# Performance work log

Measured on AMD Instinct MI355X. Metric: run time of the kernel, lower is better.

Reference implementation:

```python
import jax, jax.numpy as jnp
import numpy as np

E, H, FF = 1024, 16, 4096
HD = E // H
B, S = 4, 2048


def _ln(x, g, b, eps=1e-5):
    m = jnp.mean(x, axis=-1, keepdims=True)
    v = jnp.mean((x - m) ** 2, axis=-1, keepdims=True)
    return (x - m) / jnp.sqrt(v + eps) * g + b


def setup_inputs() -> dict:
    k = jax.random.key(0)
    ks = jax.random.split(k, 12)
    sd = 0.02
    return {
        "value": jax.random.normal(ks[0], (B, S, E), jnp.float32),
        "key": jax.random.normal(ks[1], (B, S, E), jnp.float32),
        "query": jax.random.normal(ks[2], (B, S, E), jnp.float32),
        "mask": jnp.ones((B, 1, 1, S), jnp.int32),
        "Wv": sd * jax.random.normal(ks[3], (E, E), jnp.float32),
        "Wk": sd * jax.random.normal(ks[4], (E, E), jnp.float32),
        "Wq": sd * jax.random.normal(ks[5], (E, E), jnp.float32),
        "Wo": sd * jax.random.normal(ks[6], (E, E), jnp.float32),
        "bo": jnp.zeros((E,), jnp.float32),
        "ln1_g": jnp.ones((E,), jnp.float32), "ln1_b": jnp.zeros((E,), jnp.float32),
        "ln2_g": jnp.ones((E,), jnp.float32), "ln2_b": jnp.zeros((E,), jnp.float32),
        "lnf_g": jnp.ones((E,), jnp.float32), "lnf_b": jnp.zeros((E,), jnp.float32),
        "W1": sd * jax.random.normal(ks[7], (E, FF), jnp.float32),
        "b1": jnp.zeros((FF,), jnp.float32),
        "W2": sd * jax.random.normal(ks[8], (FF, E), jnp.float32),
        "b2": jnp.zeros((E,), jnp.float32),
    }


def reference(value, key, query, mask, Wv, Wk, Wq, Wo, bo,
              ln1_g, ln1_b, ln2_g, ln2_b, lnf_g, lnf_b, W1, b1, W2, b2):
    N, Sq, Em = query.shape
    # pre-norms (value & key share prenorm2 params, as in the torch module)
    v = _ln(value, ln2_g, ln2_b)
    k = _ln(key, ln2_g, ln2_b)
    q = _ln(query, ln1_g, ln1_b)
    # QKV projections (no bias), split heads
    V = (v @ Wv).reshape(N, v.shape[1], H, HD)
    K = (k @ Wk).reshape(N, k.shape[1], H, HD)
    Q = (q @ Wq).reshape(N, Sq, H, HD)
    energy = jnp.einsum("nqhd,nkhd->nhqk", Q, K)  # [N,H,Sq,Sk]
    energy = jnp.where(mask == 0, jnp.float32(-1e20), energy)
    attn = jax.nn.softmax(energy / jnp.float32(HD ** 0.5), axis=-1)
    out = jnp.einsum("nhqk,nkhd->nqhd", attn, V).reshape(N, Sq, Em)
    out = out @ Wo + bo
    x = out + q  # residual (drop_path is identity in eval)
    f = _ln(x, lnf_g, lnf_b) @ W1 + b1
    f = jax.nn.gelu(f, approximate=False) @ W2 + b2
    return f + x
```

## Files before the change

### kernel.cpp

```cpp
#include <hip/hip_runtime.h>
#include <hip/hip_bf16.h>
#include <math.h>

typedef __bf16 bf16x8 __attribute__((ext_vector_type(8)));
typedef __bf16 bf16x4 __attribute__((ext_vector_type(4)));
typedef float f32x4 __attribute__((ext_vector_type(4)));

#define AS1 __attribute__((address_space(1)))
#define AS3 __attribute__((address_space(3)))

__device__ __forceinline__ void gll16(const __bf16* g, __bf16* l) {
    __builtin_amdgcn_global_load_lds((const AS1 unsigned int*)g,
                                     (AS3 unsigned int*)l, 16, 0, 0);
}

__device__ __forceinline__ unsigned pkbf(float a, float b) {
    union { __bf16 h[2]; unsigned u; } t;
    t.h[0] = (__bf16)a; t.h[1] = (__bf16)b;
    return t.u;
}

__global__ __launch_bounds__(256) void transpose_all(
    const float* __restrict__ Wq, const float* __restrict__ Wk,
    const float* __restrict__ Wv, const float* __restrict__ Wo,
    const float* __restrict__ W1, const float* __restrict__ W2,
    __bf16* __restrict__ Wqt, __bf16* __restrict__ Wkt,
    __bf16* __restrict__ Wvt, __bf16* __restrict__ Wot,
    __bf16* __restrict__ W1t, __bf16* __restrict__ W2t) {
    int g = blockIdx.x;
    const float* W; __bf16* Wt; int K, N, kt, nt;
    if (g < 4096) {
        int mi = g >> 10, loc = g & 1023;
        K = 1024; N = 1024; kt = loc >> 5; nt = loc & 31;
        W  = mi == 0 ? Wq  : mi == 1 ? Wk  : mi == 2 ? Wv  : Wo;
        Wt = mi == 0 ? Wqt : mi == 1 ? Wkt : mi == 2 ? Wvt : Wot;
    } else if (g < 8192) {
        int loc = g - 4096; W = W1; Wt = W1t;
        K = 1024; N = 4096; kt = loc >> 7; nt = loc & 127;
    } else {
        int loc = g - 8192; W = W2; Wt = W2t;
        K = 4096; N = 1024; kt = loc >> 5; nt = loc & 31;
    }
    int k0 = kt * 32, n0 = nt * 32;
    __shared__ float tile[32][33];
    int tx = threadIdx.x & 31, ty = threadIdx.x >> 5;
    #pragma unroll
    for (int j = ty; j < 32; j += 8)
        tile[j][tx] = W[(size_t)(k0 + j) * N + n0 + tx];
    __syncthreads();
    #pragma unroll
    for (int j = ty; j < 32; j += 8)
        Wt[(size_t)(n0 + j) * K + k0 + tx] = (__bf16)tile[tx][j];
}

__global__ __launch_bounds__(256) void ln3_kernel(
    const float* __restrict__ q, const float* __restrict__ k,
    const float* __restrict__ v,
    const float* __restrict__ g1, const float* __restrict__ b1,
    const float* __restrict__ g2, const float* __restrict__ b2,
    float* __restrict__ qln, __bf16* __restrict__ qbf,
    __bf16* __restrict__ kbf, __bf16* __restrict__ vbf) {
    const int E = 1024;
    int which = blockIdx.y;
    const float* x = which == 0 ? q : which == 1 ? k : v;
    const float* g = which == 0 ? g1 : g2;
    const float* bb = which == 0 ? b1 : b2;
    float* o32 = which == 0 ? qln : nullptr;
    __bf16* obf = which == 0 ? qbf : which == 1 ? kbf : vbf;

    size_t row = blockIdx.x;
    int t = threadIdx.x;
    float4 val = ((const float4*)(x + row * E))[t];
    float s  = val.x + val.y + val.z + val.w;
    float s2 = val.x * val.x + val.y * val.y + val.z * val.z + val.w * val.w;
    #pragma unroll
    for (int off = 32; off >= 1; off >>= 1) {
        s  += __shfl_down(s, off);
        s2 += __shfl_down(s2, off);
    }
    __shared__ float red[2][4];
    int wid = t >> 6, lane = t & 63;
    if (lane == 0) { red[0][wid] = s; red[1][wid] = s2; }
    __syncthreads();
    if (t == 0) {
        float S1 = red[0][0] + red[0][1] + red[0][2] + red[0][3];
        float S2 = red[1][0] + red[1][1] + red[1][2] + red[1][3];
        float mean = S1 / E;
        float var  = S2 / E - mean * mean;
        red[0][0] = mean;
        red[1][0] = 1.0f / sqrtf(var + 1e-5f);
    }
    __syncthreads();
    float mean = red[0][0], rstd = red[1][0];
    float4 gv = ((const float4*)g)[t];
    float4 bv = ((const float4*)bb)[t];
    float y0 = (val.x - mean) * rstd * gv.x + bv.x;
    float y1 = (val.y - mean) * rstd * gv.y + bv.y;
    float y2 = (val.z - mean) * rstd * gv.z + bv.z;
    float y3 = (val.w - mean) * rstd * gv.w + bv.w;
    if (o32) ((float4*)(o32 + row * E))[t] = make_float4(y0, y1, y2, y3);
    bf16x4 o;
    o[0] = (__bf16)y0; o[1] = (__bf16)y1; o[2] = (__bf16)y2; o[3] = (__bf16)y3;
    ((bf16x4*)(obf + row * E))[t] = o;
}

__global__ __launch_bounds__(256) void ln_kernel(const float* __restrict__ x,
                                                 const float* __restrict__ g,
                                                 const float* __restrict__ bb,
                                                 __bf16* __restrict__ outbf) {
    const int E = 1024;
    size_t row = blockIdx.x;
    int t = threadIdx.x;
    float4 v = ((const float4*)(x + row * E))[t];
    float s  = v.x + v.y + v.z + v.w;
    float s2 = v.x * v.x + v.y * v.y + v.z * v.z + v.w * v.w;
    #pragma unroll
    for (int off = 32; off >= 1; off >>= 1) {
        s  += __shfl_down(s, off);
        s2 += __shfl_down(s2, off);
    }
    __shared__ float red[2][4];
    int wid = t >> 6, lane = t & 63;
    if (lane == 0) { red[0][wid] = s; red[1][wid] = s2; }
    __syncthreads();
    if (t == 0) {
        float S1 = red[0][0] + red[0][1] + red[0][2] + red[0][3];
        float S2 = red[1][0] + red[1][1] + red[1][2] + red[1][3];
        float mean = S1 / E;
        float var  = S2 / E - mean * mean;
        red[0][0] = mean;
        red[1][0] = 1.0f / sqrtf(var + 1e-5f);
    }
    __syncthreads();
    float mean = red[0][0], rstd = red[1][0];
    float4 gv = ((const float4*)g)[t];
    float4 bv = ((const float4*)bb)[t];
    bf16x4 o;
    o[0] = (__bf16)((v.x - mean) * rstd * gv.x + bv.x);
    o[1] = (__bf16)((v.y - mean) * rstd * gv.y + bv.y);
    o[2] = (__bf16)((v.z - mean) * rstd * gv.z + bv.z);
    o[3] = (__bf16)((v.w - mean) * rstd * gv.w + bv.w);
    ((bf16x4*)(outbf + row * E))[t] = o;
}

template <int EPI>
__global__ __launch_bounds__(256) void gemm128(const __bf16* __restrict__ A,
                                               const __bf16* __restrict__ A2,
                                               const __bf16* __restrict__ Bt,
                                               const __bf16* __restrict__ Bt2,
                                               const float* __restrict__ bias,
                                               const float* __restrict__ resid,
                                               void* __restrict__ Cout,
                                               int M, int N, int K,
                                               int splitN, float scale) {
    __shared__ __bf16 As[128 * 64];
    __shared__ __bf16 Bs[128 * 64];
    int tid  = threadIdx.x;
    int lane = tid & 63, wid = tid >> 6;
    int quad = lane >> 4, l15 = lane & 15;
    int waveM = wid >> 1, waveN = wid & 1;
    size_t rowBase = (size_t)blockIdx.y * 128;
    size_t colBase = (size_t)blockIdx.x * 128;

    const __bf16* Ap = A; const __bf16* Bp = Bt;
    size_t colLoc = colBase;
    float sc = scale;
    if ((int)colBase >= splitN) { Ap = A2; Bp = Bt2; colLoc = colBase - splitN; sc = 1.0f; }

    int lrow8  = lane >> 3;
    int lchunk = (lane & 7) ^ lrow8;
    const __bf16* Ag0 = Ap + (rowBase + wid * 32 + lrow8) * (size_t)K + lchunk * 8;
    const __bf16* Bg0 = Bp + (colLoc  + wid * 32 + lrow8) * (size_t)K + lchunk * 8;
    __bf16* AsB = &As[(wid * 32) * 64];
    __bf16* BsB = &Bs[(wid * 32) * 64];

    f32x4 acc[4][4] = {};
    int swz = l15 & 7;

    for (int kb = 0; kb < K; kb += 64) {
        __syncthreads();
        #pragma unroll
        for (int i = 0; i < 4; i++) {
            gll16(Ag0 + (size_t)i * 8 * K + kb, AsB + i * 512);
            gll16(Bg0 + (size_t)i * 8 * K + kb, BsB + i * 512);
        }
        __syncthreads();
        #pragma unroll
        for (int ks = 0; ks < 2; ks++) {
            int p = ((ks * 4 + quad) ^ swz) * 8;
            bf16x8 af[4], bfr[4];
            #pragma unroll
            for (int mi = 0; mi < 4; mi++)
                af[mi] = *(const bf16x8*)&As[(waveM * 64 + mi * 16 + l15) * 64 + p];
            #pragma unroll
            for (int ni = 0; ni < 4; ni++)
                bfr[ni] = *(const bf16x8*)&Bs[(waveN * 64 + ni * 16 + l15) * 64 + p];
            #pragma unroll
            for (int mi = 0; mi < 4; mi++)
                #pragma unroll
                for (int ni = 0; ni < 4; ni++)
                    acc[mi][ni] = __builtin_amdgcn_mfma_f32_16x16x32_bf16(
                        bfr[ni], af[mi], acc[mi][ni], 0, 0, 0);
        }
    }

    #pragma unroll
    for (int mi = 0; mi < 4; mi++)
    #pragma unroll
    for (int ni = 0; ni < 4; ni++) {
        size_t row = rowBase + waveM * 64 + mi * 16 + l15;
        size_t col = colBase + waveN * 64 + ni * 16 + quad * 4;
        f32x4 v = acc[mi][ni];
        if (EPI == 1) {
            float4 b4 = *(const float4*)&bias[col];
            float4 r4 = *(const float4*)&resid[row * N + col];
            float4 o;
            o.x = v[0] + b4.x + r4.x; o.y = v[1] + b4.y + r4.y;
            o.z = v[2] + b4.z + r4.z; o.w = v[3] + b4.w + r4.w;
            *(float4*)&((float*)Cout)[row * N + col] = o;
        } else if (EPI == 2) {
            float4 b4 = *(const float4*)&bias[col];
            bf16x4 pk;
            #pragma unroll
            for (int r = 0; r < 4; r++) {
                float t2 = v[r] + ((const float*)&b4)[r];
                pk[r] = (__bf16)(0.5f * t2 * (1.0f + erff(t2 * 0.70710678118654752f)));
            }
            *(bf16x4*)&((__bf16*)Cout)[row * N + col] = pk;
        } else {
            bf16x4 pk;
            #pragma unroll
            for (int r = 0; r < 4; r++) pk[r] = (__bf16)(v[r] * sc);
            *(bf16x4*)&((__bf16*)Cout)[row * N + col] = pk;
        }
    }
}

__global__ __launch_bounds__(256) void gemmV(const __bf16* __restrict__ A,
                                             const __bf16* __restrict__ Bt,
                                             __bf16* __restrict__ Cout,
                                             int M, int N, int K) {
    __shared__ __bf16 As[128 * 64];
    __shared__ __bf16 Bs[128 * 64];
    int tid  = threadIdx.x;
    int lane = tid & 63, wid = tid >> 6;
    int quad = lane >> 4, l15 = lane & 15;
    int waveM = wid >> 1, waveN = wid & 1;
    size_t rowBase = (size_t)blockIdx.y * 128;
    size_t colBase = (size_t)blockIdx.x * 128;

    int lrow8  = lane >> 3;
    int lchunk = (lane & 7) ^ lrow8;
    const __bf16* Ag0 = A  + (rowBase + wid * 32 + lrow8) * (size_t)K + lchunk * 8;
    const __bf16* Bg0 = Bt + (colBase + wid * 32 + lrow8) * (size_t)K + lchunk * 8;
    __bf16* AsB = &As[(wid * 32) * 64];
    __bf16* BsB = &Bs[(wid * 32) * 64];

    f32x4 acc[4][4] = {};
    int swz = l15 & 7;

    for (int kb = 0; kb < K; kb += 64) {
        __syncthreads();
        #pragma unroll
        for (int i = 0; i < 4; i++) {
            gll16(Ag0 + (size_t)i * 8 * K + kb, AsB + i * 512);
            gll16(Bg0 + (size_t)i * 8 * K + kb, BsB + i * 512);
        }
        __syncthreads();
        #pragma unroll
        for (int ks = 0; ks < 2; ks++) {
            int p = ((ks * 4 + quad) ^ swz) * 8;
            bf16x8 af[4], bfr[4];
            #pragma unroll
            for (int mi = 0; mi < 4; mi++)
                af[mi] = *(const bf16x8*)&As[(waveM * 64 + mi * 16 + l15) * 64 + p];
            #pragma unroll
            for (int ni = 0; ni < 4; ni++)
                bfr[ni] = *(const bf16x8*)&Bs[(waveN * 64 + ni * 16 + l15) * 64 + p];
            #pragma unroll
            for (int mi = 0; mi < 4; mi++)
                #pragma unroll
                for (int ni = 0; ni < 4; ni++)
                    acc[mi][ni] = __builtin_amdgcn_mfma_f32_16x16x32_bf16(
                        af[mi], bfr[ni], acc[mi][ni], 0, 0, 0);
        }
    }

    #pragma unroll
    for (int mi = 0; mi < 4; mi++)
    #pragma unroll
    for (int ni = 0; ni < 4; ni++) {
        size_t col = colBase + waveN * 64 + ni * 16 + l15;
        size_t m0  = rowBase + waveM * 64 + mi * 16 + quad * 4;
        bf16x4 pk;
        #pragma unroll
        for (int r = 0; r < 4; r++) pk[r] = (__bf16)acc[mi][ni][r];
        *(bf16x4*)&Cout[col * M + m0] = pk;
    }
}

__global__ __launch_bounds__(256) void attn_kernel(const __bf16* __restrict__ QK,
                                                   const __bf16* __restrict__ Vt,
                                                   const int* __restrict__ mask,
                                                   __bf16* __restrict__ Out) {
    const int S = 2048, E = 1024, E2 = 2048, M = 8192;
    int qt = blockIdx.x, bh = blockIdx.y;
    int b = bh >> 4, h = bh & 15;
    int q0 = qt * 128;
    int tid = threadIdx.x, lane = tid & 63, wid = tid >> 6;
    int quad = lane >> 4, l15 = lane & 15;

    __shared__ __bf16 KV[2][2 * 4096];

    bf16x8 aq[2][2];
    #pragma unroll
    for (int m = 0; m < 2; m++)
        #pragma unroll
        for (int hh = 0; hh < 2; hh++) {
            size_t row = (size_t)(b * S + q0 + wid * 32 + m * 16 + l15);
            aq[m][hh] = *(const bf16x8*)(QK + row * E2 + h * 64 + hh * 32 + quad * 8);
        }

    int lrow8  = lane >> 3;
    int lchunk = (lane & 7) ^ lrow8;
    const __bf16* Kg0 = QK + (size_t)(b * S + wid * 16 + lrow8) * E2 + 1024 + h * 64 + lchunk * 8;
    const __bf16* Vg0 = Vt + (size_t)(h * 64 + wid * 16 + lrow8) * M + b * S + lchunk * 8;

    int srcA = ((quad & 1) * 2) * 16 + l15;
    int srcB = srcA + 16;
    bool selHi = (quad >= 2);
    int swz = l15 & 7;

    f32x4 accO[2][4] = {};
    float accl[2] = {0.f, 0.f};

    {
        __bf16* Kd = &KV[0][(wid * 16) * 64];
        __bf16* Vd = &KV[0][4096 + (wid * 16) * 64];
        #pragma unroll
        for (int i = 0; i < 2; i++) {
            gll16(Kg0 + (size_t)i * 8 * E2, Kd + i * 512);
            gll16(Vg0 + (size_t)i * 8 * M,  Vd + i * 512);
        }
    }
    __syncthreads();

    for (int kt = 0; kt < S / 64; kt++) {
        int k0 = kt * 64;
        int buf = kt & 1;
        if (kt + 1 < S / 64) {
            int kn = k0 + 64;
            __bf16* Kd = &KV[buf ^ 1][(wid * 16) * 64];
            __bf16* Vd = &KV[buf ^ 1][4096 + (wid * 16) * 64];
            #pragma unroll
            for (int i = 0; i < 2; i++) {
                gll16(Kg0 + (size_t)(kn + i * 8) * E2, Kd + i * 512);
                gll16(Vg0 + (size_t)i * 8 * M + kn,    Vd + i * 512);
            }
        }
        const __bf16* Ksb = &KV[buf][0];
        const __bf16* Vsb = &KV[buf][4096];

        f32x4 sa[2][4];
        #pragma unroll
        for (int nt = 0; nt < 4; nt++) {
            bf16x8 a0 = *(const bf16x8*)&Ksb[(nt * 16 + l15) * 64 + ((0 * 4 + quad) ^ swz) * 8];
            bf16x8 a1 = *(const bf16x8*)&Ksb[(nt * 16 + l15) * 64 + ((1 * 4 + quad) ^ swz) * 8];
            #pragma unroll
            for (int m = 0; m < 2; m++) {
                f32x4 a = {};
                a = __builtin_amdgcn_mfma_f32_16x16x32_bf16(a0, aq[m][0], a, 0, 0, 0);
                a = __builtin_amdgcn_mfma_f32_16x16x32_bf16(a1, aq[m][1], a, 0, 0, 0);
                sa[m][nt] = a;
            }
        }

        unsigned pd[2][4][2];
        #pragma unroll
        for (int nt = 0; nt < 4; nt++) {
            int4 mz = *(const int4*)&mask[b * S + k0 + nt * 16 + quad * 4];
            #pragma unroll
            for (int m = 0; m < 2; m++) {
                float p0 = mz.x ? __expf(sa[m][nt][0]) : 0.f;
                float p1 = mz.y ? __expf(sa[m][nt][1]) : 0.f;
                float p2 = mz.z ? __expf(sa[m][nt][2]) : 0.f;
                float p3 = mz.w ? __expf(sa[m][nt][3]) : 0.f;
                accl[m] += (p0 + p1) + (p2 + p3);
                pd[m][nt][0] = pkbf(p0, p1);
                pd[m][nt][1] = pkbf(p2, p3);
            }
        }

        bf16x8 bfrag[2][2];
        #pragma unroll
        for (int m = 0; m < 2; m++)
            #pragma unroll
            for (int hh = 0; hh < 2; hh++) {
                int ntLo = 2 * hh;
                unsigned dA0 = __shfl((int)pd[m][ntLo][0], srcA, 64);
                unsigned dB0 = __shfl((int)pd[m][ntLo + 1][0], srcA, 64);
                unsigned dA1 = __shfl((int)pd[m][ntLo][1], srcA, 64);
                unsigned dB1 = __shfl((int)pd[m][ntLo + 1][1], srcA, 64);
                unsigned dA2 = __shfl((int)pd[m][ntLo][0], srcB, 64);
                unsigned dB2 = __shfl((int)pd[m][ntLo + 1][0], srcB, 64);
                unsigned dA3 = __shfl((int)pd[m][ntLo][1], srcB, 64);
                unsigned dB3 = __shfl((int)pd[m][ntLo + 1][1], srcB, 64);
                union { unsigned u[4]; bf16x8 v; } w;
                w.u[0] = selHi ? dB0 : dA0;
                w.u[1] = selHi ? dB1 : dA1;
                w.u[2] = selHi ? dB2 : dA2;
                w.u[3] = selHi ? dB3 : dA3;
                bfrag[m][hh] = w.v;
            }

        #pragma unroll
        for (int dt = 0; dt < 4; dt++) {
            bf16x8 v0 = *(const bf16x8*)&Vsb[(dt * 16 + l15) * 64 + ((0 * 4 + quad) ^ swz) * 8];
            bf16x8 v1 = *(const bf16x8*)&Vsb[(dt * 16 + l15) * 64 + ((1 * 4 + quad) ^ swz) * 8];
            #pragma unroll
            for (int m = 0; m < 2; m++) {
                accO[m][dt] = __builtin_amdgcn_mfma_f32_16x16x32_bf16(v0, bfrag[m][0], accO[m][dt], 0, 0, 0);
                accO[m][dt] = __builtin_amdgcn_mfma_f32_16x16x32_bf16(v1, bfrag[m][1], accO[m][dt], 0, 0, 0);
            }
        }
        __syncthreads();
    }

    float inv[2];
    #pragma unroll
    for (int m = 0; m < 2; m++) {
        float l = accl[m];
        l += __shfl_xor(l, 16, 64);
        l += __shfl_xor(l, 32, 64);
        inv[m] = 1.0f / l;
    }

    #pragma unroll
    for (int m = 0; m < 2; m++)
        #pragma unroll
        for (int dt = 0; dt < 4; dt++) {
            size_t row = (size_t)(b * S + q0 + wid * 32 + m * 16 + l15);
            bf16x4 pk;
            #pragma unroll
            for (int r = 0; r < 4; r++) pk[r] = (__bf16)(accO[m][dt][r] * inv[m]);
            *(bf16x4*)&Out[row * E + h * 64 + dt * 16 + quad * 4] = pk;
        }
}

extern "C" void kernel_launch(void* const* d_in, const int* in_sizes, int n_in,
                              void* d_out, int out_size, void* d_ws, size_t ws_size,
                              hipStream_t stream) {
    const int Bb = 4, S = 2048, E = 1024, FF = 4096;
    const int M = Bb * S;

    const float* value = (const float*)d_in[0];
    const float* key   = (const float*)d_in[1];
    const float* query = (const float*)d_in[2];
    const int*   mask  = (const int*)d_in[3];
    const float* Wv    = (const float*)d_in[4];
    const float* Wk    = (const float*)d_in[5];
    const float* Wq    = (const float*)d_in[6];
    const float* Wo    = (const float*)d_in[7];
    const float* bo    = (const float*)d_in[8];
    const float* ln1_g = (const float*)d_in[9];
    const float* ln1_b = (const float*)d_in[10];
    const float* ln2_g = (const float*)d_in[11];
    const float* ln2_b = (const float*)d_in[12];
    const float* lnf_g = (const float*)d_in[13];
    const float* lnf_b = (const float*)d_in[14];
    const float* W1    = (const float*)d_in[15];
    const float* b1    = (const float*)d_in[16];
    const float* W2    = (const float*)d_in[17];
    const float* b2    = (const float*)d_in[18];

    char* ws = (char*)d_ws;
    const size_t MB = 1024 * 1024;
    __bf16* Wqt = (__bf16*)(ws + 0 * MB);
    __bf16* Wkt = (__bf16*)(ws + 2 * MB);
    __bf16* Wvt = (__bf16*)(ws + 4 * MB);
    __bf16* Wot = (__bf16*)(ws + 6 * MB);
    __bf16* W1t = (__bf16*)(ws + 8 * MB);
    __bf16* W2t = (__bf16*)(ws + 16 * MB);
    __bf16* q_bf = (__bf16*)(ws + 24 * MB);
    __bf16* k_bf = (__bf16*)(ws + 40 * MB);
    __bf16* v_bf = (__bf16*)(ws + 56 * MB);
    __bf16* QKb  = (__bf16*)(ws + 72 * MB);
    __bf16* Vtg  = (__bf16*)(ws + 104 * MB);
    __bf16* attn = q_bf;
    __bf16* x_ln = k_bf;
    __bf16* h1   = v_bf;
    float*  qln  = (float*)(ws + 120 * MB);
    float*  x32  = (float*)(ws + 152 * MB);

    transpose_all<<<12288, 256, 0, stream>>>(Wq, Wk, Wv, Wo, W1, W2,
                                             Wqt, Wkt, Wvt, Wot, W1t, W2t);

    ln3_kernel<<<dim3(M, 3), 256, 0, stream>>>(query, key, value,
                                               ln1_g, ln1_b, ln2_g, ln2_b,
                                               qln, q_bf, k_bf, v_bf);

    gemm128<0><<<dim3(2 * E / 128, M / 128), 256, 0, stream>>>(
        q_bf, k_bf, Wqt, Wkt, nullptr, nullptr, QKb, M, 2 * E, E, E, 0.125f);

    gemmV<<<dim3(E / 128, M / 128), 256, 0, stream>>>(v_bf, Wvt, Vtg, M, E, E);

    attn_kernel<<<dim3(S / 128, Bb * 16), 256, 0, stream>>>(QKb, Vtg, mask, attn);

    gemm128<1><<<dim3(E / 128, M / 128), 256, 0, stream>>>(
        attn, attn, Wot, Wot, bo, qln, x32, M, E, E, E, 1.0f);

    ln_kernel<<<M, 256, 0, stream>>>(x32, lnf_g, lnf_b, x_ln);

    gemm128<2><<<dim3(FF / 128, M / 128), 256, 0, stream>>>(
        x_ln, x_ln, W1t, W1t, b1, nullptr, h1, M, FF, E, FF, 1.0f);
    gemm128<1><<<dim3(E / 128, M / 128), 256, 0, stream>>>(
        h1, h1, W2t, W2t, b2, x32, (float*)d_out, M, E, FF, E, 1.0f);
}
```

Baseline: 721.1 us.

## Fuse QKV GEMMs, shrink attention per-wave rows, use 128x64 tiles for N=1024 GEMMs

Q, K and V projections now run in one launch that picks its input and weight by column segment, with V still written transposed. The attention kernel moves to 512 threads, each wave owning 16 query rows instead of 32, and launch_bounds(512,6) is meant to raise occupancy and cut register pressure. The output and FFN-down GEMMs use 128x64 tiles to double the block count for N=1024. The costs are more K/V tile loads per query, smaller per-block reuse in those GEMMs, and a branch inside the fused QKV kernel.

```diff
diff --git a/kernel.cpp b/kernel.cpp
--- a/kernel.cpp
+++ b/kernel.cpp
@@ -143,73 +143,66 @@
     ((bf16x4*)(outbf + row * E))[t] = o;
 }
 
-template <int EPI>
-__global__ __launch_bounds__(256) void gemm128(const __bf16* __restrict__ A,
-                                               const __bf16* __restrict__ A2,
+template <int EPI, int TMD, int TND>
+__global__ __launch_bounds__(256) void gemm_tn(const __bf16* __restrict__ A,
                                                const __bf16* __restrict__ Bt,
-                                               const __bf16* __restrict__ Bt2,
                                                const float* __restrict__ bias,
                                                const float* __restrict__ resid,
                                                void* __restrict__ Cout,
-                                               int M, int N, int K,
-                                               int splitN, float scale) {
-    __shared__ __bf16 As[128 * 64];
-    __shared__ __bf16 Bs[128 * 64];
+                                               int M, int N, int K) {
+    __shared__ __bf16 As[TMD * 32 * 64];
+    __shared__ __bf16 Bs[TND * 32 * 64];
     int tid  = threadIdx.x;
     int lane = tid & 63, wid = tid >> 6;
     int quad = lane >> 4, l15 = lane & 15;
     int waveM = wid >> 1, waveN = wid & 1;
-    size_t rowBase = (size_t)blockIdx.y * 128;
-    size_t colBase = (size_t)blockIdx.x * 128;
-
-    const __bf16* Ap = A; const __bf16* Bp = Bt;
-    size_t colLoc = colBase;
-    float sc = scale;
-    if ((int)colBase >= splitN) { Ap = A2; Bp = Bt2; colLoc = colBase - splitN; sc = 1.0f; }
+    size_t rowBase = (size_t)blockIdx.y * (TMD * 32);
+    size_t colBase = (size_t)blockIdx.x * (TND * 32);
 
     int lrow8  = lane >> 3;
     int lchunk = (lane & 7) ^ lrow8;
-    const __bf16* Ag0 = Ap + (rowBase + wid * 32 + lrow8) * (size_t)K + lchunk * 8;
-    const __bf16* Bg0 = Bp + (colLoc  + wid * 32 + lrow8) * (size_t)K + lchunk * 8;
-    __bf16* AsB = &As[(wid * 32) * 64];
-    __bf16* BsB = &Bs[(wid * 32) * 64];
-
-    f32x4 acc[4][4] = {};
+    const __bf16* Ag0 = A  + (rowBase + wid * (8 * TMD) + lrow8) * (size_t)K + lchunk * 8;
+    const __bf16* Bg0 = Bt + (colBase + wid * (8 * TND) + lrow8) * (size_t)K + lchunk * 8;
+    __bf16* AsB = &As[(wid * 8 * TMD) * 64];
+    __bf16* BsB = &Bs[(wid * 8 * TND) * 64];
+
+    f32x4 acc[TMD][TND] = {};
     int swz = l15 & 7;
 
     for (int kb = 0; kb < K; kb += 64) {
         __syncthreads();
         #pragma unroll
-        for (int i = 0; i < 4; i++) {
+        for (int i = 0; i < TMD; i++)
             gll16(Ag0 + (size_t)i * 8 * K + kb, AsB + i * 512);
+        #pragma unroll
+        for (int i = 0; i < TND; i++)
             gll16(Bg0 + (size_t)i * 8 * K + kb, BsB + i * 512);
-        }
         __syncthreads();
         #pragma unroll
         for (int ks = 0; ks < 2; ks++) {
             int p = ((ks * 4 + quad) ^ swz) * 8;
-            bf16x8 af[4], bfr[4];
-            #pragma unroll
-            for (int mi = 0; mi < 4; mi++)
-                af[mi] = *(const bf16x8*)&As[(waveM * 64 + mi * 16 + l15) * 64 + p];
-            #pragma unroll
-            for (int ni = 0; ni < 4; ni++)
-                bfr[ni] = *(const bf16x8*)&Bs[(waveN * 64 + ni * 16 + l15) * 64 + p];
-            #pragma unroll
-            for (int mi = 0; mi < 4; mi++)
+            bf16x8 af[TMD], bfr[TND];
+            #pragma unroll
+            for (int mi = 0; mi < TMD; mi++)
+                af[mi] = *(const bf16x8*)&As[(waveM * 16 * TMD + mi * 16 + l15) * 64 + p];
+            #pragma unroll
+            for (int ni = 0; ni < TND; ni++)
+                bfr[ni] = *(const bf16x8*)&Bs[(waveN * 16 * TND + ni * 16 + l15) * 64 + p];
+            #pragma unroll
+            for (int mi = 0; mi < TMD; mi++)
                 #pragma unroll
-                for (int ni = 0; ni < 4; ni++)
+                for (int ni = 0; ni < TND; ni++)
                     acc[mi][ni] = __builtin_amdgcn_mfma_f32_16x16x32_bf16(
                         bfr[ni], af[mi], acc[mi][ni], 0, 0, 0);
         }
     }
 
     #pragma unroll
-    for (int mi = 0; mi < 4; mi++)
-    #pragma unroll
-    for (int ni = 0; ni < 4; ni++) {
-        size_t row = rowBase + waveM * 64 + mi * 16 + l15;
-        size_t col = colBase + waveN * 64 + ni * 16 + quad * 4;
+    for (int mi = 0; mi < TMD; mi++)
+    #pragma unroll
+    for (int ni = 0; ni < TND; ni++) {
+        size_t row = rowBase + waveM * 16 * TMD + mi * 16 + l15;
+        size_t col = colBase + waveN * 16 * TND + ni * 16 + quad * 4;
         f32x4 v = acc[mi][ni];
         if (EPI == 1) {
             float4 b4 = *(const float4*)&bias[col];
@@ -218,7 +211,7 @@
             o.x = v[0] + b4.x + r4.x; o.y = v[1] + b4.y + r4.y;
             o.z = v[2] + b4.z + r4.z; o.w = v[3] + b4.w + r4.w;
             *(float4*)&((float*)Cout)[row * N + col] = o;
-        } else if (EPI == 2) {
+        } else {
             float4 b4 = *(const float4*)&bias[col];
             bf16x4 pk;
             #pragma unroll
@@ -227,19 +220,19 @@
                 pk[r] = (__bf16)(0.5f * t2 * (1.0f + erff(t2 * 0.70710678118654752f)));
             }
             *(bf16x4*)&((__bf16*)Cout)[row * N + col] = pk;
-        } else {
-            bf16x4 pk;
-            #pragma unroll
-            for (int r = 0; r < 4; r++) pk[r] = (__bf16)(v[r] * sc);
-            *(bf16x4*)&((__bf16*)Cout)[row * N + col] = pk;
-        }
-    }
-}
-
-__global__ __launch_bounds__(256) void gemmV(const __bf16* __restrict__ A,
-                                             const __bf16* __restrict__ Bt,
-                                             __bf16* __restrict__ Cout,
-                                             int M, int N, int K) {
+        }
+    }
+}
+
+__global__ __launch_bounds__(256) void gemm_qkv(const __bf16* __restrict__ qbf,
+                                                const __bf16* __restrict__ kbf,
+                                                const __bf16* __restrict__ vbf,
+                                                const __bf16* __restrict__ Wqt,
+                                                const __bf16* __restrict__ Wkt,
+                                                const __bf16* __restrict__ Wvt,
+                                                __bf16* __restrict__ QKb,
+                                                __bf16* __restrict__ Vtg,
+                                                int M, int K) {
     __shared__ __bf16 As[128 * 64];
     __shared__ __bf16 Bs[128 * 64];
     int tid  = threadIdx.x;
@@ -247,12 +240,16 @@
     int quad = lane >> 4, l15 = lane & 15;
     int waveM = wid >> 1, waveN = wid & 1;
     size_t rowBase = (size_t)blockIdx.y * 128;
-    size_t colBase = (size_t)blockIdx.x * 128;
+    int seg = blockIdx.x >> 3;
+    size_t colLoc = (size_t)(blockIdx.x & 7) * 128;
+
+    const __bf16* Ap = seg == 0 ? qbf : seg == 1 ? kbf : vbf;
+    const __bf16* Bp = seg == 0 ? Wqt : seg == 1 ? Wkt : Wvt;
 
     int lrow8  = lane >> 3;
     int lchunk = (lane & 7) ^ lrow8;
-    const __bf16* Ag0 = A  + (rowBase + wid * 32 + lrow8) * (size_t)K + lchunk * 8;
-    const __bf16* Bg0 = Bt + (colBase + wid * 32 + lrow8) * (size_t)K + lchunk * 8;
+    const __bf16* Ag0 = Ap + (rowBase + wid * 32 + lrow8) * (size_t)K + lchunk * 8;
+    const __bf16* Bg0 = Bp + (colLoc  + wid * 32 + lrow8) * (size_t)K + lchunk * 8;
     __bf16* AsB = &As[(wid * 32) * 64];
     __bf16* BsB = &Bs[(wid * 32) * 64];
 
@@ -277,32 +274,56 @@
             #pragma unroll
             for (int ni = 0; ni < 4; ni++)
                 bfr[ni] = *(const bf16x8*)&Bs[(waveN * 64 + ni * 16 + l15) * 64 + p];
-            #pragma unroll
-            for (int mi = 0; mi < 4; mi++)
+            if (seg != 2) {
                 #pragma unroll
-                for (int ni = 0; ni < 4; ni++)
-                    acc[mi][ni] = __builtin_amdgcn_mfma_f32_16x16x32_bf16(
-                        af[mi], bfr[ni], acc[mi][ni], 0, 0, 0);
-        }
-    }
-
-    #pragma unroll
-    for (int mi = 0; mi < 4; mi++)
-    #pragma unroll
-    for (int ni = 0; ni < 4; ni++) {
-        size_t col = colBase + waveN * 64 + ni * 16 + l15;
-        size_t m0  = rowBase + waveM * 64 + mi * 16 + quad * 4;
-        bf16x4 pk;
-        #pragma unroll
-        for (int r = 0; r < 4; r++) pk[r] = (__bf16)acc[mi][ni][r];
-        *(bf16x4*)&Cout[col * M + m0] = pk;
-    }
-}
-
-__global__ __launch_bounds__(256) void attn_kernel(const __bf16* __restrict__ QK,
-                                                   const __bf16* __restrict__ Vt,
-                                                   const int* __restrict__ mask,
-                                                   __bf16* __restrict__ Out) {
+                for (int mi = 0; mi < 4; mi++)
+                    #pragma unroll
+                    for (int ni = 0; ni < 4; ni++)
+                        acc[mi][ni] = __builtin_amdgcn_mfma_f32_16x16x32_bf16(
+                            bfr[ni], af[mi], acc[mi][ni], 0, 0, 0);
+            } else {
+                #pragma unroll
+                for (int mi = 0; mi < 4; mi++)
+                    #pragma unroll
+                    for (int ni = 0; ni < 4; ni++)
+                        acc[mi][ni] = __builtin_amdgcn_mfma_f32_16x16x32_bf16(
+                            af[mi], bfr[ni], acc[mi][ni], 0, 0, 0);
+            }
+        }
+    }
+
+    if (seg != 2) {
+        float sc = seg == 0 ? 0.125f : 1.0f;
+        #pragma unroll
+        for (int mi = 0; mi < 4; mi++)
+        #pragma unroll
+        for (int ni = 0; ni < 4; ni++) {
+            size_t row = rowBase + waveM * 64 + mi * 16 + l15;
+            size_t col = (size_t)seg * 1024 + colLoc + waveN * 64 + ni * 16 + quad * 4;
+            bf16x4 pk;
+            #pragma unroll
+            for (int r = 0; r < 4; r++) pk[r] = (__bf16)(acc[mi][ni][r] * sc);
+            *(bf16x4*)&QKb[row * 2048 + col] = pk;
+        }
+    } else {
+        #pragma unroll
+        for (int mi = 0; mi < 4; mi++)
+        #pragma unroll
+        for (int ni = 0; ni < 4; ni++) {
+            size_t col = colLoc + waveN * 64 + ni * 16 + l15;
+            size_t m0  = rowBase + waveM * 64 + mi * 16 + quad * 4;
+            bf16x4 pk;
+            #pragma unroll
+            for (int r = 0; r < 4; r++) pk[r] = (__bf16)acc[mi][ni][r];
+            *(bf16x4*)&Vtg[col * M + m0] = pk;
+        }
+    }
+}
+
+__global__ __launch_bounds__(512, 6) void attn_kernel(const __bf16* __restrict__ QK,
+                                                      const __bf16* __restrict__ Vt,
+                                                      const int* __restrict__ mask,
+                                                      __bf16* __restrict__ Out) {
     const int S = 2048, E = 1024, E2 = 2048, M = 8192;
     int qt = blockIdx.x, bh = blockIdx.y;
     int b = bh >> 4, h = bh & 15;
@@ -312,37 +333,28 @@
 
     __shared__ __bf16 KV[2][2 * 4096];
 
-    bf16x8 aq[2][2];
-    #pragma unroll
-    for (int m = 0; m < 2; m++)
-        #pragma unroll
-        for (int hh = 0; hh < 2; hh++) {
-            size_t row = (size_t)(b * S + q0 + wid * 32 + m * 16 + l15);
-            aq[m][hh] = *(const bf16x8*)(QK + row * E2 + h * 64 + hh * 32 + quad * 8);
-        }
+    bf16x8 aq[2];
+    #pragma unroll
+    for (int hh = 0; hh < 2; hh++) {
+        size_t row = (size_t)(b * S + q0 + wid * 16 + l15);
+        aq[hh] = *(const bf16x8*)(QK + row * E2 + h * 64 + hh * 32 + quad * 8);
+    }
 
     int lrow8  = lane >> 3;
     int lchunk = (lane & 7) ^ lrow8;
-    const __bf16* Kg0 = QK + (size_t)(b * S + wid * 16 + lrow8) * E2 + 1024 + h * 64 + lchunk * 8;
-    const __bf16* Vg0 = Vt + (size_t)(h * 64 + wid * 16 + lrow8) * M + b * S + lchunk * 8;
+    const __bf16* Kg0 = QK + (size_t)(b * S + wid * 8 + lrow8) * E2 + 1024 + h * 64 + lchunk * 8;
+    const __bf16* Vg0 = Vt + (size_t)(h * 64 + wid * 8 + lrow8) * M + b * S + lchunk * 8;
 
     int srcA = ((quad & 1) * 2) * 16 + l15;
     int srcB = srcA + 16;
     bool selHi = (quad >= 2);
     int swz = l15 & 7;
 
-    f32x4 accO[2][4] = {};
-    float accl[2] = {0.f, 0.f};
-
-    {
-        __bf16* Kd = &KV[0][(wid * 16) * 64];
-        __bf16* Vd = &KV[0][4096 + (wid * 16) * 64];
-        #pragma unroll
-        for (int i = 0; i < 2; i++) {
-            gll16(Kg0 + (size_t)i * 8 * E2, Kd + i * 512);
-            gll16(Vg0 + (size_t)i * 8 * M,  Vd + i * 512);
-        }
-    }
+    f32x4 accO[4] = {};
+    float accl = 0.f;
+
+    gll16(Kg0, &KV[0][wid * 512]);
+    gll16(Vg0, &KV[0][4096 + wid * 512]);
     __syncthreads();
 
     for (int kt = 0; kt < S / 64; kt++) {
@@ -350,101 +362,79 @@
         int buf = kt & 1;
         if (kt + 1 < S / 64) {
             int kn = k0 + 64;
-            __bf16* Kd = &KV[buf ^ 1][(wid * 16) * 64];
-            __bf16* Vd = &KV[buf ^ 1][4096 + (wid * 16) * 64];
-            #pragma unroll
-            for (int i = 0; i < 2; i++) {
-                gll16(Kg0 + (size_t)(kn + i * 8) * E2, Kd + i * 512);
-                gll16(Vg0 + (size_t)i * 8 * M + kn,    Vd + i * 512);
-            }
+            gll16(Kg0 + (size_t)kn * E2, &KV[buf ^ 1][wid * 512]);
+            gll16(Vg0 + kn,              &KV[buf ^ 1][4096 + wid * 512]);
         }
         const __bf16* Ksb = &KV[buf][0];
         const __bf16* Vsb = &KV[buf][4096];
 
-        f32x4 sa[2][4];
+        f32x4 sa[4];
         #pragma unroll
         for (int nt = 0; nt < 4; nt++) {
-            bf16x8 a0 = *(const bf16x8*)&Ksb[(nt * 16 + l15) * 64 + ((0 * 4 + quad) ^ swz) * 8];
-            bf16x8 a1 = *(const bf16x8*)&Ksb[(nt * 16 + l15) * 64 + ((1 * 4 + quad) ^ swz) * 8];
-            #pragma unroll
-            for (int m = 0; m < 2; m++) {
-                f32x4 a = {};
-                a = __builtin_amdgcn_mfma_f32_16x16x32_bf16(a0, aq[m][0], a, 0, 0, 0);
-                a = __builtin_amdgcn_mfma_f32_16x16x32_bf16(a1, aq[m][1], a, 0, 0, 0);
-                sa[m][nt] = a;
-            }
-        }
-
-        unsigned pd[2][4][2];
+            bf16x8 a0 = *(const bf16x8*)&Ksb[(nt * 16 + l15) * 64 + ((quad) ^ swz) * 8];
+            bf16x8 a1 = *(const bf16x8*)&Ksb[(nt * 16 + l15) * 64 + ((4 + quad) ^ swz) * 8];
+            f32x4 a = {};
+            a = __builtin_amdgcn_mfma_f32_16x16x32_bf16(a0, aq[0], a, 0, 0, 0);
+            a = __builtin_amdgcn_mfma_f32_16x16x32_bf16(a1, aq[1], a, 0, 0, 0);
+            sa[nt] = a;
+        }
+
+        unsigned pd[4][2];
         #pragma unroll
         for (int nt = 0; nt < 4; nt++) {
             int4 mz = *(const int4*)&mask[b * S + k0 + nt * 16 + quad * 4];
-            #pragma unroll
-            for (int m = 0; m < 2; m++) {
-                float p0 = mz.x ? __expf(sa[m][nt][0]) : 0.f;
-                float p1 = mz.y ? __expf(sa[m][nt][1]) : 0.f;
-                float p2 = mz.z ? __expf(sa[m][nt][2]) : 0.f;
-                float p3 = mz.w ? __expf(sa[m][nt][3]) : 0.f;
-                accl[m] += (p0 + p1) + (p2 + p3);
-                pd[m][nt][0] = pkbf(p0, p1);
-                pd[m][nt][1] = pkbf(p2, p3);
-            }
-        }
-
-        bf16x8 bfrag[2][2];
-        #pragma unroll
-        for (int m = 0; m < 2; m++)
-            #pragma unroll
-            for (int hh = 0; hh < 2; hh++) {
-                int ntLo = 2 * hh;
-                unsigned dA0 = __shfl((int)pd[m][ntLo][0], srcA, 64);
-                unsigned dB0 = __shfl((int)pd[m][ntLo + 1][0], srcA, 64);
-                unsigned dA1 = __shfl((int)pd[m][ntLo][1], srcA, 64);
-                unsigned dB1 = __shfl((int)pd[m][ntLo + 1][1], srcA, 64);
-                unsigned dA2 = __shfl((int)pd[m][ntLo][0], srcB, 64);
-                unsigned dB2 = __shfl((int)pd[m][ntLo + 1][0], srcB, 64);
-                unsigned dA3 = __shfl((int)pd[m][ntLo][1], srcB, 64);
-                unsigned dB3 = __shfl((int)pd[m][ntLo + 1][1], srcB, 64);
-                union { unsigned u[4]; bf16x8 v; } w;
-                w.u[0] = selHi ? dB0 : dA0;
-                w.u[1] = selHi ? dB1 : dA1;
-                w.u[2] = selHi ? dB2 : dA2;
-                w.u[3] = selHi ? dB3 : dA3;
-                bfrag[m][hh] = w.v;
-            }
+            float p0 = mz.x ? __expf(sa[nt][0]) : 0.f;
+            float p1 = mz.y ? __expf(sa[nt][1]) : 0.f;
+            float p2 = mz.z ? __expf(sa[nt][2]) : 0.f;
+            float p3 = mz.w ? __expf(sa[nt][3]) : 0.f;
+            accl += (p0 + p1) + (p2 + p3);
+            pd[nt][0] = pkbf(p0, p1);
+            pd[nt][1] = pkbf(p2, p3);
+        }
+
+        bf16x8 bfrag[2];
+        #pragma unroll
+        for (int hh = 0; hh < 2; hh++) {
+            int ntLo = 2 * hh;
+            unsigned dA0 = __shfl((int)pd[ntLo][0], srcA, 64);
+            unsigned dB0 = __shfl((int)pd[ntLo + 1][0], srcA, 64);
+            unsigned dA1 = __shfl((int)pd[ntLo][1], srcA, 64);
+            unsigned dB1 = __shfl((int)pd[ntLo + 1][1], srcA, 64);
+            unsigned dA2 = __shfl((int)pd[ntLo][0], srcB, 64);
+            unsigned dB2 = __shfl((int)pd[ntLo + 1][0], srcB, 64);
+            unsigned dA3 = __shfl((int)pd[ntLo][1], srcB, 64);
+            unsigned dB3 = __shfl((int)pd[ntLo + 1][1], srcB, 64);
+            union { unsigned u[4]; bf16x8 v; } w;
+            w.u[0] = selHi ? dB0 : dA0;
+            w.u[1] = selHi ? dB1 : dA1;
+            w.u[2] = selHi ? dB2 : dA2;
+            w.u[3] = selHi ? dB3 : dA3;
+            bfrag[hh] = w.v;
+        }
 
         #pragma unroll
         for (int dt = 0; dt < 4; dt++) {
-            bf16x8 v0 = *(const bf16x8*)&Vsb[(dt * 16 + l15) * 64 + ((0 * 4 + quad) ^ swz) * 8];
-            bf16x8 v1 = *(const bf16x8*)&Vsb[(dt * 16 + l15) * 64 + ((1 * 4 + quad) ^ swz) * 8];
-            #pragma unroll
-            for (int m = 0; m < 2; m++) {
-                accO[m][dt] = __builtin_amdgcn_mfma_f32_16x16x32_bf16(v0, bfrag[m][0], accO[m][dt], 0, 0, 0);
-                accO[m][dt] = __builtin_amdgcn_mfma_f32_16x16x32_bf16(v1, bfrag[m][1], accO[m][dt], 0, 0, 0);
-            }
+            bf16x8 v0 = *(const bf16x8*)&Vsb[(dt * 16 + l15) * 64 + ((quad) ^ swz) * 8];
+            bf16x8 v1 = *(const bf16x8*)&Vsb[(dt * 16 + l15) * 64 + ((4 + quad) ^ swz) * 8];
+            accO[dt] = __builtin_amdgcn_mfma_f32_16x16x32_bf16(v0, bfrag[0], accO[dt], 0, 0, 0);
+            accO[dt] = __builtin_amdgcn_mfma_f32_16x16x32_bf16(v1, bfrag[1], accO[dt], 0, 0, 0);
         }
         __syncthreads();
     }
 
-    float inv[2];
-    #pragma unroll
-    for (int m = 0; m < 2; m++) {
-        float l = accl[m];
-        l += __shfl_xor(l, 16, 64);
-        l += __shfl_xor(l, 32, 64);
-        inv[m] = 1.0f / l;
-    }
-
-    #pragma unroll
-    for (int m = 0; m < 2; m++)
-        #pragma unroll
-        for (int dt = 0; dt < 4; dt++) {
-            size_t row = (size_t)(b * S + q0 + wid * 32 + m * 16 + l15);
-            bf16x4 pk;
-            #pragma unroll
-            for (int r = 0; r < 4; r++) pk[r] = (__bf16)(accO[m][dt][r] * inv[m]);
-            *(bf16x4*)&Out[row * E + h * 64 + dt * 16 + quad * 4] = pk;
-        }
+    float l = accl;
+    l += __shfl_xor(l, 16, 64);
+    l += __shfl_xor(l, 32, 64);
+    float inv = 1.0f / l;
+
+    #pragma unroll
+    for (int dt = 0; dt < 4; dt++) {
+        size_t row = (size_t)(b * S + q0 + wid * 16 + l15);
+        bf16x4 pk;
+        #pragma unroll
+        for (int r = 0; r < 4; r++) pk[r] = (__bf16)(accO[dt][r] * inv);
+        *(bf16x4*)&Out[row * E + h * 64 + dt * 16 + quad * 4] = pk;
+    }
 }
 
 extern "C" void kernel_launch(void* const* d_in, const int* in_sizes, int n_in,
@@ -499,20 +489,18 @@
                                                ln1_g, ln1_b, ln2_g, ln2_b,
                                                qln, q_bf, k_bf, v_bf);
 
-    gemm128<0><<<dim3(2 * E / 128, M / 128), 256, 0, stream>>>(
-        q_bf, k_bf, Wqt, Wkt, nullptr, nullptr, QKb, M, 2 * E, E, E, 0.125f);
-
-    gemmV<<<dim3(E / 128, M / 128), 256, 0, stream>>>(v_bf, Wvt, Vtg, M, E, E);
-
-    attn_kernel<<<dim3(S / 128, Bb * 16), 256, 0, stream>>>(QKb, Vtg, mask, attn);
-
-    gemm128<1><<<dim3(E / 128, M / 128), 256, 0, stream>>>(
-        attn, attn, Wot, Wot, bo, qln, x32, M, E, E, E, 1.0f);
+    gemm_qkv<<<dim3(24, M / 128), 256, 0, stream>>>(q_bf, k_bf, v_bf,
+                                                    Wqt, Wkt, Wvt, QKb, Vtg, M, E);
+
+    attn_kernel<<<dim3(S / 128, Bb * 16), 512, 0, stream>>>(QKb, Vtg, mask, attn);
+
+    gemm_tn<1, 4, 2><<<dim3(E / 64, M / 128), 256, 0, stream>>>(
+        attn, Wot, bo, qln, x32, M, E, E);
 
     ln_kernel<<<M, 256, 0, stream>>>(x32, lnf_g, lnf_b, x_ln);
 
-    gemm128<2><<<dim3(FF / 128, M / 128), 256, 0, stream>>>(
-        x_ln, x_ln, W1t, W1t, b1, nullptr, h1, M, FF, E, FF, 1.0f);
-    gemm128<1><<<dim3(E / 128, M / 128), 256, 0, stream>>>(
-        h1, h1, W2t, W2t, b2, x32, (float*)d_out, M, E, FF, E, 1.0f);
-}
+    gemm_tn<2, 4, 4><<<dim3(FF / 128, M / 128), 256, 0, stream>>>(
+        x_ln, W1t, b1, nullptr, h1, M, FF, E);
+    gemm_tn<1, 4, 2><<<dim3(E / 64, M / 128), 256, 0, stream>>>(
+        h1, W2t, b2, x32, (float*)d_out, M, E, FF);
+}
```

Result: slower. 759.0 us (+5.3%).
